# Kernel optimization log

Measured on AMD Instinct MI355X. Metric: run time of the kernel, lower is better.

Reference implementation:

```python
import jax, jax.numpy as jnp
import numpy as np

GAMMA = 0.01      # rbf gamma (init kwarg)
C = 10            # n_classes (len(nv))
NV = 500          # support vectors per class (equal segments)
# all (i, j) class pairs with i < j, in the original nested-loop order
PAIRS = np.array([(i, j) for i in range(C) for j in range(i + 1, C)], dtype=np.int32)
I_IDX = jnp.asarray(PAIRS[:, 0])  # [45]
J_IDX = jnp.asarray(PAIRS[:, 1])  # [45]


def setup_inputs() -> dict:
    key = jax.random.key(0)
    k1, k2, k3, k4 = jax.random.split(key, 4)
    x = jax.random.normal(k1, (8192, 256), dtype=jnp.float32)
    sv = jax.random.normal(k2, (5000, 256), dtype=jnp.float32)
    a = jax.random.normal(k3, (C - 1, 5000), dtype=jnp.float32) * 0.1  # dual coefs
    b = jax.random.normal(k4, (45,), dtype=jnp.float32) * 0.1          # intercepts per pair
    return {"x": x, "sv": sv, "a": a, "b": b}


def reference(x, sv, a, b):
    # RBF kernel matrix: k[n, s] = exp(-gamma * ||x_n - sv_s||^2)
    x_norm = jnp.sum(x * x, axis=1)[:, None]            # [N, 1]
    sv_norm = jnp.sum(sv * sv, axis=1)[None, :]         # [1, SV]
    k = jnp.exp(-GAMMA * (x_norm + sv_norm) + 2.0 * GAMMA * (x @ sv.T))  # [N, SV]

    N = x.shape[0]
    kr = k.reshape(N, C, NV)           # per-class SV segments
    ar = a.reshape(C - 1, C, NV)       # dual coef rows, segmented the same way
    # T[n, r, c] = sum_m a[r, segment c, m] * k[n, segment c, m]
    # (fuses every inner Python loop of the original into one contraction)
    T = jnp.einsum('ncm,rcm->nrc', kr, ar)              # [N, C-1, C]

    # decision for pair (i, j): a[i, seg j] . k_seg_j + a[j-1, seg i] . k_seg_i + b
    c = T[:, I_IDX, J_IDX] + T[:, J_IDX - 1, I_IDX] + b[None, :]  # [N, 45]

    # pairwise voting: winner i if c > 0 else j; class id = mode of votes
    votes = jnp.where(c > 0, I_IDX[None, :], J_IDX[None, :])      # [N, 45] int32
    counts = jnp.sum(jax.nn.one_hot(votes, C, dtype=jnp.float32), axis=1)  # [N, C]
    # argmax picks the smallest class index on ties, matching torch.mode
    class_ids = jnp.argmax(counts, axis=1).astype(jnp.int32)
    return (class_ids, class_ids)
```

## Files before the change

kernel.cpp:

```cpp
#include <hip/hip_runtime.h>
#include <hip/hip_fp16.h>
#include <cmath>


#define GAMMA 0.01f
constexpr int N  = 8192;
constexpr int D  = 256;
constexpr int S  = 5000;
constexpr int C  = 10;
constexpr int NV = 500;
constexpr int R  = 9;
constexpr int SPAD = 5120;

constexpr int ROW_BLOCKS = (N + S) / 4;
constexpr int A_BLOCKS   = (16 * SPAD) / 256;

typedef _Float16 f16x8 __attribute__((ext_vector_type(8)));
typedef _Float16 f16x4 __attribute__((ext_vector_type(4)));
typedef float    f32x4 __attribute__((ext_vector_type(4)));

__device__ __forceinline__ void gload16(const void* g, void* l) {
    __builtin_amdgcn_global_load_lds(
        (const __attribute__((address_space(1))) void*)g,
        (__attribute__((address_space(3))) void*)l, 16, 0, 0);
}

__global__ __launch_bounds__(256) void prep_kernel(const float* __restrict__ x,
                                                   const float* __restrict__ sv,
                                                   const float* __restrict__ a,
                                                   _Float16* __restrict__ xth,
                                                   _Float16* __restrict__ xtl,
                                                   _Float16* __restrict__ sh,
                                                   _Float16* __restrict__ sl,
                                                   float* __restrict__ xn,
                                                   _Float16* __restrict__ ah,
                                                   _Float16* __restrict__ al,
                                                   float* __restrict__ svnp) {
    if (blockIdx.x >= ROW_BLOCKS) {
        int idx = (blockIdx.x - ROW_BLOCKS) * 256 + threadIdx.x;
        int r = idx / SPAD, col = idx - r * SPAD;
        int cls = col >> 9, j = col & 511;
        int s = cls * NV + ((j < NV) ? j : NV - 1);
        float av = (r < R && j < NV) ? a[(size_t)r * S + s] : 0.0f;
        _Float16 h = (_Float16)av;
        ah[idx] = h;
        al[idx] = (_Float16)((av - (float)h) * 4096.0f);
        return;
    }
    int gid  = blockIdx.x * blockDim.x + threadIdx.x;
    int wid  = gid >> 6;
    int lane = gid & 63;
    bool isx = wid < N;
    int  r   = isx ? wid : wid - N;
    const float* row = isx ? (x + (size_t)r * D) : (sv + (size_t)r * D);
    float4 v = reinterpret_cast<const float4*>(row)[lane];
    float s = v.x * v.x + v.y * v.y + v.z * v.z + v.w * v.w;
#pragma unroll
    for (int off = 32; off > 0; off >>= 1) s += __shfl_xor(s, off, 64);
    float vv[4] = {v.x, v.y, v.z, v.w};
    f16x4 h, l;
#pragma unroll
    for (int k = 0; k < 4; ++k) {
        _Float16 hi = (_Float16)vv[k];
        h[k] = hi;
        l[k] = (_Float16)((vv[k] - (float)hi) * 4096.0f);
    }
    if (isx) {
        size_t xt = (((size_t)(r >> 4) * 8 + (lane >> 3)) * 4 + ((lane >> 1) & 3)) * 128
                  + (size_t)(r & 15) * 8 + (lane & 1) * 4;
        *(f16x4*)(xth + xt) = h;
        *(f16x4*)(xtl + xt) = l;
    } else {
        size_t o = (size_t)r * D + lane * 4;
        *(f16x4*)(sh + o) = h;
        *(f16x4*)(sl + o) = l;
    }
    if (lane == 0) {
        if (isx) {
            xn[r] = s;
        } else {
            int cls = r / NV, j = r - cls * NV;
            svnp[cls * 512 + j] = s;
            if (j == NV - 1)
                for (int p = NV; p < 512; ++p) svnp[cls * 512 + p] = s;
        }
    }
}

__global__ __launch_bounds__(256, 3) void svc_gemm(const _Float16* __restrict__ xth,
                                                   const _Float16* __restrict__ xtl,
                                                   const _Float16* __restrict__ sh,
                                                   const _Float16* __restrict__ sl,
                                                   const _Float16* __restrict__ ahp,
                                                   const _Float16* __restrict__ alp,
                                                   const float* __restrict__ xnorm,
                                                   const float* __restrict__ svnp,
                                                   float* __restrict__ T) {
    __shared__ _Float16 SVs[2][2][128 * 32];

    const int tid  = threadIdx.x;
    const int n0   = blockIdx.x * 64;
    const int cls  = blockIdx.y;
    const int w    = tid >> 6;
    const int lane = tid & 63;
    const int wm   = w >> 1;
    const int wn   = w & 1;
    const int lx   = lane & 15;
    const int quad = lane >> 4;

    float xnr[2];
#pragma unroll
    for (int nt = 0; nt < 2; ++nt)
        xnr[nt] = xnorm[n0 + wn * 32 + nt * 16 + lx];

    int svoff[4];
#pragma unroll
    for (int mt = 0; mt < 4; ++mt) {
        int row = wm * 64 + mt * 16 + lx;
        svoff[mt] = row * 32 + ((quad - (row >> 1)) & 3) * 8;
    }

    const int arow = tid >> 2, ag = tid & 3;
    const int sg   = (ag + (arow >> 1)) & 3;
    const int segend = cls * NV + NV - 1;
    const int ldsw = w * 512;

    auto stage = [&](int ph, int buf) {
        const int ch = ph >> 3, kb = ph & 7;
        const size_t koff = (size_t)(kb * 32 + sg * 8);
        const int svbase = cls * NV + ch * 128;
        int svr0 = svbase + arow;      if (svr0 > segend) svr0 = segend;
        int svr1 = svbase + arow + 64; if (svr1 > segend) svr1 = segend;
        const size_t go0 = (size_t)svr0 * D + koff;
        const size_t go1 = (size_t)svr1 * D + koff;
        gload16(sh + go0, &SVs[buf][0][ldsw]);
        gload16(sl + go0, &SVs[buf][1][ldsw]);
        gload16(sh + go1, &SVs[buf][0][2048 + ldsw]);
        gload16(sl + go1, &SVs[buf][1][2048 + ldsw]);
    };

    const int pn0 = blockIdx.x * 4 + wn * 2;
    const size_t xq = (size_t)quad * 128 + (size_t)lx * 8;
    f16x8 pBE[2][2], pBO[2][2];
    auto loadB = [&](f16x8 (&dst)[2][2], int kb) {
        const size_t o0 = ((size_t)(pn0 * 8 + kb) * 4) * 128 + xq;
        const size_t o1 = ((size_t)((pn0 + 1) * 8 + kb) * 4) * 128 + xq;
        dst[0][0] = *(const f16x8*)(xth + o0);
        dst[1][0] = *(const f16x8*)(xtl + o0);
        dst[0][1] = *(const f16x8*)(xth + o1);
        dst[1][1] = *(const f16x8*)(xtl + o1);
    };

    f32x4 accM[4][2], accC[4][2];
#pragma unroll
    for (int mt = 0; mt < 4; ++mt)
#pragma unroll
        for (int nt = 0; nt < 2; ++nt) {
            accM[mt][nt] = (f32x4){0.f, 0.f, 0.f, 0.f};
            accC[mt][nt] = (f32x4){0.f, 0.f, 0.f, 0.f};
        }
    f32x4 accO[2], accOC[2];
#pragma unroll
    for (int nt = 0; nt < 2; ++nt) {
        accO[nt]  = (f32x4){0.f, 0.f, 0.f, 0.f};
        accOC[nt] = (f32x4){0.f, 0.f, 0.f, 0.f};
    }

    auto compute = [&](int buf, const f16x8 (&pB)[2][2]) {
        f16x8 Am[2][4];
#pragma unroll
        for (int mt = 0; mt < 4; ++mt) {
            Am[0][mt] = *(const f16x8*)(&SVs[buf][0][svoff[mt]]);
            Am[1][mt] = *(const f16x8*)(&SVs[buf][1][svoff[mt]]);
        }
        __builtin_amdgcn_s_setprio(1);
#pragma unroll
        for (int mt = 0; mt < 4; ++mt)
#pragma unroll
            for (int nt = 0; nt < 2; ++nt) {
                accM[mt][nt] = __builtin_amdgcn_mfma_f32_16x16x32_f16(
                    Am[0][mt], pB[0][nt], accM[mt][nt], 0, 0, 0);
                accC[mt][nt] = __builtin_amdgcn_mfma_f32_16x16x32_f16(
                    Am[0][mt], pB[1][nt], accC[mt][nt], 0, 0, 0);
                accC[mt][nt] = __builtin_amdgcn_mfma_f32_16x16x32_f16(
                    Am[1][mt], pB[0][nt], accC[mt][nt], 0, 0, 0);
            }
        __builtin_amdgcn_s_setprio(0);
    };

    auto epilogue = [&](int ch) {
        const int mbase = cls * 512 + ch * 128 + wm * 64;
#pragma unroll
        for (int mt = 0; mt < 4; ++mt) {
            const size_t ao = (size_t)lx * SPAD + mbase + mt * 16 + quad * 4;
            f16x4 afh = *(const f16x4*)(ahp + ao);
            f16x4 afl = *(const f16x4*)(alp + ao);
            float4 sn4 = *(const float4*)(svnp + mbase + mt * 16 + quad * 4);
#pragma unroll
            for (int nt = 0; nt < 2; ++nt) {
                f16x4 bh, bl;
#pragma unroll
                for (int reg = 0; reg < 4; ++reg) {
                    float dot = accM[mt][nt][reg]
                              + accC[mt][nt][reg] * (1.0f / 4096.0f);
                    float e  = fmaf(2.0f * GAMMA, dot,
                                    -GAMMA * (xnr[nt] + sn4[reg]));
                    float kv = __expf(e);
                    _Float16 h = (_Float16)kv;
                    bh[reg] = h;
                    bl[reg] = (_Float16)((kv - (float)h) * 4096.0f);
                }
                accO[nt]  = __builtin_amdgcn_mfma_f32_16x16x16f16(
                    afh, bh, accO[nt], 0, 0, 0);
                accOC[nt] = __builtin_amdgcn_mfma_f32_16x16x16f16(
                    afh, bl, accOC[nt], 0, 0, 0);
                accOC[nt] = __builtin_amdgcn_mfma_f32_16x16x16f16(
                    afl, bh, accOC[nt], 0, 0, 0);
                accM[mt][nt] = (f32x4){0.f, 0.f, 0.f, 0.f};
                accC[mt][nt] = (f32x4){0.f, 0.f, 0.f, 0.f};
            }
        }
    };

    stage(0, 0);
    loadB(pBE, 0);

    for (int it = 0; it < 16; ++it) {
        asm volatile("s_waitcnt lgkmcnt(0)" ::: "memory");
        asm volatile("s_waitcnt vmcnt(4)" ::: "memory");
        __builtin_amdgcn_s_barrier();
        asm volatile("" ::: "memory");
        stage(2 * it + 1, 1);
        loadB(pBO, (2 * it + 1) & 7);
        compute(0, pBE);
        asm volatile("s_waitcnt lgkmcnt(0)" ::: "memory");
        asm volatile("s_waitcnt vmcnt(4)" ::: "memory");
        __builtin_amdgcn_s_barrier();
        asm volatile("" ::: "memory");
        if (it < 15) {
            stage(2 * it + 2, 0);
            loadB(pBE, (2 * it + 2) & 7);
        }
        compute(1, pBO);
        if ((it & 3) == 3) epilogue(it >> 2);
    }

    float* scr = (float*)&SVs[0][0][0];
    __syncthreads();
    if (wm == 0) {
#pragma unroll
        for (int nt = 0; nt < 2; ++nt)
#pragma unroll
            for (int reg = 0; reg < 4; ++reg) {
                int base = ((wn * 2 + nt) * 2) * 256 + (quad * 4 + reg) * 16 + lx;
                scr[base]       = accO[nt][reg];
                scr[base + 256] = accOC[nt][reg];
            }
    }
    __syncthreads();
    if (wm == 1) {
#pragma unroll
        for (int nt = 0; nt < 2; ++nt)
#pragma unroll
            for (int reg = 0; reg < 4; ++reg) {
                int r = quad * 4 + reg;
                if (r < R) {
                    int base = ((wn * 2 + nt) * 2) * 256 + r * 16 + lx;
                    float o  = accO[nt][reg]  + scr[base];
                    float oc = accOC[nt][reg] + scr[base + 256];
                    int n = n0 + wn * 32 + nt * 16 + lx;
                    T[(size_t)(r * 10 + cls) * N + n] = o + oc * (1.0f / 4096.0f);
                }
            }
    }
}

__global__ __launch_bounds__(256) void vote_kernel(const float* __restrict__ T,
                                                   const float* __restrict__ b,
                                                   int* __restrict__ out) {
    int n = blockIdx.x * blockDim.x + threadIdx.x;
    if (n >= N) return;
    float tv[90];
#pragma unroll
    for (int i = 0; i < 90; ++i) tv[i] = T[(size_t)i * N + n];
    int counts[C];
#pragma unroll
    for (int k = 0; k < C; ++k) counts[k] = 0;
    int p = 0;
#pragma unroll
    for (int i = 0; i < C; ++i) {
#pragma unroll
        for (int j = i + 1; j < C; ++j) {
            float c = tv[i * 10 + j] + tv[(j - 1) * 10 + i] + b[p];
            if (c > 0.f) counts[i]++; else counts[j]++;
            ++p;
        }
    }
    int best = 0;
#pragma unroll
    for (int k = 1; k < C; ++k)
        if (counts[k] > counts[best]) best = k;
    out[n]     = best;
    out[N + n] = best;
}

extern "C" void kernel_launch(void* const* d_in, const int* in_sizes, int n_in,
                              void* d_out, int out_size, void* d_ws, size_t ws_size,
                              hipStream_t stream) {
    const float* x  = (const float*)d_in[0];
    const float* sv = (const float*)d_in[1];
    const float* a  = (const float*)d_in[2];
    const float* b  = (const float*)d_in[3];
    int* out = (int*)d_out;

    char* wp = (char*)d_ws;
    _Float16* xth = (_Float16*)wp; wp += (size_t)N * D * 2;
    _Float16* xtl = (_Float16*)wp; wp += (size_t)N * D * 2;
    _Float16* sh  = (_Float16*)wp; wp += (size_t)S * D * 2;
    _Float16* sl  = (_Float16*)wp; wp += (size_t)S * D * 2;
    float* xnorm  = (float*)wp;    wp += (size_t)N * 4;
    _Float16* ahp = (_Float16*)wp; wp += (size_t)16 * SPAD * 2;
    _Float16* alp = (_Float16*)wp; wp += (size_t)16 * SPAD * 2;
    float* svnp   = (float*)wp;    wp += (size_t)SPAD * 4;
    float* T      = (float*)wp;

    {
        prep_kernel<<<ROW_BLOCKS + A_BLOCKS, 256, 0, stream>>>(
            x, sv, a, xth, xtl, sh, sl, xnorm, ahp, alp, svnp);
    }
    {
        dim3 grid(N / 64, C);
        svc_gemm<<<grid, 256, 0, stream>>>(xth, xtl, sh, sl, ahp, alp,
                                           xnorm, svnp, T);
    }
    {
        vote_kernel<<<N / 256, 256, 0, stream>>>(T, b, out);
    }
}
```

Baseline: 165.7 us.

## Shrink GEMM blocks to two waves and drop cross-wave LDS reduction

```diff
diff --git a/kernel.cpp b/kernel.cpp
--- a/kernel.cpp
+++ b/kernel.cpp
@@ -87,7 +87,7 @@
     }
 }
 
-__global__ __launch_bounds__(256, 3) void svc_gemm(const _Float16* __restrict__ xth,
+__global__ __launch_bounds__(128, 3) void svc_gemm(const _Float16* __restrict__ xth,
                                                    const _Float16* __restrict__ xtl,
                                                    const _Float16* __restrict__ sh,
                                                    const _Float16* __restrict__ sl,
@@ -96,27 +96,25 @@
                                                    const float* __restrict__ xnorm,
                                                    const float* __restrict__ svnp,
                                                    float* __restrict__ T) {
-    __shared__ _Float16 SVs[2][2][128 * 32];
+    __shared__ _Float16 SVs[2][2][64 * 32];
 
     const int tid  = threadIdx.x;
     const int n0   = blockIdx.x * 64;
     const int cls  = blockIdx.y;
     const int w    = tid >> 6;
     const int lane = tid & 63;
-    const int wm   = w >> 1;
-    const int wn   = w & 1;
     const int lx   = lane & 15;
     const int quad = lane >> 4;
 
     float xnr[2];
 #pragma unroll
     for (int nt = 0; nt < 2; ++nt)
-        xnr[nt] = xnorm[n0 + wn * 32 + nt * 16 + lx];
+        xnr[nt] = xnorm[n0 + w * 32 + nt * 16 + lx];
 
     int svoff[4];
 #pragma unroll
     for (int mt = 0; mt < 4; ++mt) {
-        int row = wm * 64 + mt * 16 + lx;
+        int row = mt * 16 + lx;
         svoff[mt] = row * 32 + ((quad - (row >> 1)) & 3) * 8;
     }
 
@@ -128,18 +126,18 @@
     auto stage = [&](int ph, int buf) {
         const int ch = ph >> 3, kb = ph & 7;
         const size_t koff = (size_t)(kb * 32 + sg * 8);
-        const int svbase = cls * NV + ch * 128;
+        const int svbase = cls * NV + ch * 64;
         int svr0 = svbase + arow;      if (svr0 > segend) svr0 = segend;
-        int svr1 = svbase + arow + 64; if (svr1 > segend) svr1 = segend;
+        int svr1 = svbase + arow + 32; if (svr1 > segend) svr1 = segend;
         const size_t go0 = (size_t)svr0 * D + koff;
         const size_t go1 = (size_t)svr1 * D + koff;
         gload16(sh + go0, &SVs[buf][0][ldsw]);
         gload16(sl + go0, &SVs[buf][1][ldsw]);
-        gload16(sh + go1, &SVs[buf][0][2048 + ldsw]);
-        gload16(sl + go1, &SVs[buf][1][2048 + ldsw]);
+        gload16(sh + go1, &SVs[buf][0][1024 + ldsw]);
+        gload16(sl + go1, &SVs[buf][1][1024 + ldsw]);
     };
 
-    const int pn0 = blockIdx.x * 4 + wn * 2;
+    const int pn0 = blockIdx.x * 4 + w * 2;
     const size_t xq = (size_t)quad * 128 + (size_t)lx * 8;
     f16x8 pBE[2][2], pBO[2][2];
     auto loadB = [&](f16x8 (&dst)[2][2], int kb) {
@@ -189,7 +187,7 @@
     };
 
     auto epilogue = [&](int ch) {
-        const int mbase = cls * 512 + ch * 128 + wm * 64;
+        const int mbase = cls * 512 + ch * 64;
 #pragma unroll
         for (int mt = 0; mt < 4; ++mt) {
             const size_t ao = (size_t)lx * SPAD + mbase + mt * 16 + quad * 4;
@@ -225,7 +223,7 @@
     stage(0, 0);
     loadB(pBE, 0);
 
-    for (int it = 0; it < 16; ++it) {
+    for (int it = 0; it < 32; ++it) {
         asm volatile("s_waitcnt lgkmcnt(0)" ::: "memory");
         asm volatile("s_waitcnt vmcnt(4)" ::: "memory");
         __builtin_amdgcn_s_barrier();
@@ -237,7 +235,7 @@
         asm volatile("s_waitcnt vmcnt(4)" ::: "memory");
         __builtin_amdgcn_s_barrier();
         asm volatile("" ::: "memory");
-        if (it < 15) {
+        if (it < 31) {
             stage(2 * it + 2, 0);
             loadB(pBE, (2 * it + 2) & 7);
         }
@@ -245,34 +243,17 @@
         if ((it & 3) == 3) epilogue(it >> 2);
     }
 
-    float* scr = (float*)&SVs[0][0][0];
-    __syncthreads();
-    if (wm == 0) {
-#pragma unroll
-        for (int nt = 0; nt < 2; ++nt)
-#pragma unroll
-            for (int reg = 0; reg < 4; ++reg) {
-                int base = ((wn * 2 + nt) * 2) * 256 + (quad * 4 + reg) * 16 + lx;
-                scr[base]       = accO[nt][reg];
-                scr[base + 256] = accOC[nt][reg];
+#pragma unroll
+    for (int nt = 0; nt < 2; ++nt)
+#pragma unroll
+        for (int reg = 0; reg < 4; ++reg) {
+            int r = quad * 4 + reg;
+            if (r < R) {
+                int n = n0 + w * 32 + nt * 16 + lx;
+                T[(size_t)(r * 10 + cls) * N + n] =
+                    accO[nt][reg] + accOC[nt][reg] * (1.0f / 4096.0f);
             }
-    }
-    __syncthreads();
-    if (wm == 1) {
-#pragma unroll
-        for (int nt = 0; nt < 2; ++nt)
-#pragma unroll
-            for (int reg = 0; reg < 4; ++reg) {
-                int r = quad * 4 + reg;
-                if (r < R) {
-                    int base = ((wn * 2 + nt) * 2) * 256 + r * 16 + lx;
-                    float o  = accO[nt][reg]  + scr[base];
-                    float oc = accOC[nt][reg] + scr[base + 256];
-                    int n = n0 + wn * 32 + nt * 16 + lx;
-                    T[(size_t)(r * 10 + cls) * N + n] = o + oc * (1.0f / 4096.0f);
-                }
-            }
-    }
+        }
 }
 
 __global__ __launch_bounds__(256) void vote_kernel(const float* __restrict__ T,
@@ -330,7 +311,7 @@
     }
     {
         dim3 grid(N / 64, C);
-        svc_gemm<<<grid, 256, 0, stream>>>(xth, xtl, sh, sl, ahp, alp,
+        svc_gemm<<<grid, 128, 0, stream>>>(xth, xtl, sh, sl, ahp, alp,
                                            xnorm, svnp, T);
     }
     {
```

Result: slower. 169.9 us (+2.5%).
